# Performance work log

Measured on AMD Instinct MI355X. Metric: run time of the kernel, lower is better.

## Reference

```python
import jax, jax.numpy as jnp
import numpy as np

N, E, G = 100000, 800000, 64
F_IN, H = 92, 4
D1, D2, D3 = 32, 64, 128  # per-head out dims: hidden//2, hidden, 2*hidden
HID, LAT = 64, 128
FINAL = H * D3  # 512
NEG_SLOPE = 0.2


def _p(key, shape, scale=0.05):
    return jax.random.normal(key, shape, dtype=jnp.float32) * scale


def setup_inputs() -> dict:
    key = jax.random.key(0)
    ks = jax.random.split(key, 32)
    node_feat = jax.random.normal(ks[0], (N, F_IN), dtype=jnp.float32)
    src = jax.random.randint(ks[1], (E,), 0, N)
    dst = jax.random.randint(ks[2], (E,), 0, N)
    graph_id = jnp.sort(jax.random.randint(ks[3], (N,), 0, G))
    d = {"node_feat": node_feat, "src": src, "dst": dst, "graph_id": graph_id}
    # GAT layer params (DGL GATConv: fc no bias, attn_l/attn_r [H,D], bias [H*D])
    dims = [(F_IN, D1), (H * D1, D2), (H * D2, D3)]
    i = 4
    for li, (fi, do) in enumerate(dims, 1):
        d[f"W{li}"] = _p(ks[i], (fi, H * do)); i += 1
        d[f"al{li}"] = _p(ks[i], (H, do)); i += 1
        d[f"ar{li}"] = _p(ks[i], (H, do)); i += 1
        d[f"b{li}"] = jnp.zeros((H * do,), dtype=jnp.float32)
    # gate MLP: Linear(final, hid) -> ReLU -> Linear(hid, 1)
    d["Wg1"] = _p(ks[i], (FINAL, HID)); i += 1
    d["bg1"] = jnp.zeros((HID,), dtype=jnp.float32)
    d["Wg2"] = _p(ks[i], (HID, 1)); i += 1
    d["bg2"] = jnp.zeros((1,), dtype=jnp.float32)
    d["Wmu"] = _p(ks[i], (FINAL, LAT)); i += 1
    d["bmu"] = jnp.zeros((LAT,), dtype=jnp.float32)
    d["Wlv"] = _p(ks[i], (FINAL, LAT)); i += 1
    d["blv"] = jnp.zeros((LAT,), dtype=jnp.float32)
    return d


def gat_layer(h, W, al, ar, b, src, dst, heads, d_out):
    n = h.shape[0]
    Wh = (h @ W).reshape(n, heads, d_out)                      # [N,H,D]
    el = jnp.einsum('nhd,hd->nh', Wh, al)                      # a_l . Wh
    er = jnp.einsum('nhd,hd->nh', Wh, ar)
    e = jax.nn.leaky_relu(el[src] + er[dst], NEG_SLOPE)        # [E,H]
    m = jax.ops.segment_max(e, dst, num_segments=n)
    m = jnp.where(jnp.isfinite(m), m, 0.0)                     # zero-in-degree guard
    ex = jnp.exp(e - m[dst])
    s = jax.ops.segment_sum(ex, dst, num_segments=n)
    a = ex / jnp.maximum(s[dst], 1e-9)                         # edge softmax
    msg = a[:, :, None] * Wh[src]                              # [E,H,D] (peak intermediate)
    out = jax.ops.segment_sum(msg, dst, num_segments=n)        # scatter-aggregate
    out = out + b.reshape(1, heads, d_out)
    return out.reshape(n, heads * d_out)                       # flatten(1)


def attention_pool(h, graph_id, Wg1, bg1, Wg2, bg2, num_graphs):
    gate = jax.nn.relu(h @ Wg1 + bg1) @ Wg2 + bg2              # [N,1]
    m = jax.ops.segment_max(gate, graph_id, num_segments=num_graphs)
    ex = jnp.exp(gate - m[graph_id])
    s = jax.ops.segment_sum(ex, graph_id, num_segments=num_graphs)
    a = ex / jnp.maximum(s[graph_id], 1e-9)                    # softmax over nodes per graph
    return jax.ops.segment_sum(a * h, graph_id, num_segments=num_graphs)  # [G,final]


def reference(node_feat, src, dst, graph_id,
              W1, al1, ar1, b1, W2, al2, ar2, b2, W3, al3, ar3, b3,
              Wg1, bg1, Wg2, bg2, Wmu, bmu, Wlv, blv):
    h = jax.nn.elu(gat_layer(node_feat, W1, al1, ar1, b1, src, dst, H, D1))
    h = jax.nn.elu(gat_layer(h, W2, al2, ar2, b2, src, dst, H, D2))
    h = jax.nn.elu(gat_layer(h, W3, al3, ar3, b3, src, dst, H, D3))
    g = attention_pool(h, graph_id, Wg1, bg1, Wg2, bg2, G)
    mu = g @ Wmu + bmu
    logvar = g @ Wlv + blv
    return (mu, logvar)
```

## Files before the change

kernel.cpp:

```cpp
#include <hip/hip_runtime.h>
#include <math.h>

#define NNODES 100000
#define NEDGES 800000
#define NGRAPH 64
#define NHEAD  4
#define FINALD 512
#define HIDG   64
#define LATD   128
#define K1P    96
#define NB_SCAN 98
#define PQ     16

typedef unsigned int uint;
typedef unsigned short ushort;
typedef __attribute__((ext_vector_type(8))) short bf16x8;
typedef __attribute__((ext_vector_type(4))) float f32x4;

__device__ __forceinline__ float bflo(uint u) { return __uint_as_float(u << 16); }
__device__ __forceinline__ float bfhi(uint u) { return __uint_as_float(u & 0xffff0000u); }
__device__ __forceinline__ ushort f2bf(float f) {
    uint u = __float_as_uint(f);
    return (ushort)((u + 0x7fffu + ((u >> 16) & 1u)) >> 16);
}
__device__ __forceinline__ uint pack2(float a, float b) {
    return (uint)f2bf(a) | ((uint)f2bf(b) << 16);
}
__device__ __forceinline__ void fmabf2(float w, uint v, float& a0, float& a1) {
    a0 = fmaf(w, bflo(v), a0);
    a1 = fmaf(w, bfhi(v), a1);
}

__device__ __forceinline__ void async_copy16(const ushort* gsrc, ushort* lds_base) {
    __builtin_amdgcn_global_load_lds(
        (const __attribute__((address_space(1))) uint*)gsrc,
        (__attribute__((address_space(3))) uint*)lds_base,
        16, 0, 0);
}

__global__ void init_kernel(int* __restrict__ deg, const int* __restrict__ gid,
                            int* __restrict__ gstart) {
    int i = blockIdx.x * blockDim.x + threadIdx.x;
    if (i < NNODES) deg[i] = 0;
    if (i <= NGRAPH) {
        int lo = 0, hi = NNODES;
        while (lo < hi) {
            int mid = (lo + hi) >> 1;
            if (gid[mid] < i) lo = mid + 1; else hi = mid;
        }
        gstart[i] = lo;
    }
}
__global__ void count_kernel(const int* __restrict__ dst, int* __restrict__ deg) {
    int e = blockIdx.x * blockDim.x + threadIdx.x;
    if (e < NEDGES) atomicAdd(&deg[dst[e]], 1);
}
__global__ __launch_bounds__(1024) void scan_block_kernel(const int* __restrict__ deg,
                                                          int* __restrict__ off,
                                                          int* __restrict__ bsum) {
    __shared__ int buf[1024];
    int t = threadIdx.x;
    int i = blockIdx.x * 1024 + t;
    int x = (i < NNODES) ? deg[i] : 0;
    buf[t] = x;
    __syncthreads();
    for (int s = 1; s < 1024; s <<= 1) {
        int v = (t >= s) ? buf[t - s] : 0;
        __syncthreads();
        buf[t] += v;
        __syncthreads();
    }
    if (i < NNODES) off[i] = buf[t] - x;
    if (t == 1023) bsum[blockIdx.x] = buf[1023];
}
__global__ __launch_bounds__(128) void scan_bsum_kernel(int* __restrict__ bsum) {
    __shared__ int buf[128];
    int t = threadIdx.x;
    int x = (t < NB_SCAN) ? bsum[t] : 0;
    buf[t] = x;
    __syncthreads();
    for (int s = 1; s < 128; s <<= 1) {
        int v = (t >= s) ? buf[t - s] : 0;
        __syncthreads();
        buf[t] += v;
        __syncthreads();
    }
    if (t < NB_SCAN) bsum[t] = buf[t] - x;
    if (t == 0) bsum[NB_SCAN] = buf[NB_SCAN - 1];
}
__global__ __launch_bounds__(1024) void scan_add_kernel(int* __restrict__ off,
                                                        const int* __restrict__ bsum,
                                                        int* __restrict__ cursor) {
    int i = blockIdx.x * 1024 + threadIdx.x;
    if (i < NNODES) {
        int v = off[i] + bsum[blockIdx.x];
        off[i] = v;
        cursor[i] = v;
    }
    if (i == 0) off[NNODES] = bsum[NB_SCAN];
}
__global__ void scatter_kernel(const int* __restrict__ src, const int* __restrict__ dst,
                               int* __restrict__ cursor, int* __restrict__ src_csr) {
    int e = blockIdx.x * blockDim.x + threadIdx.x;
    if (e >= NEDGES) return;
    int p = atomicAdd(&cursor[dst[e]], 1);
    src_csr[p] = src[e];
}

#define C1 (128 * K1P)
#define C2 (256 * 128)
#define C3 (512 * 256)
#define CG (64 * 512)
#define CX (NNODES * K1P)
#define CTOT (C1 + C2 + C3 + CG + CX + NNODES)
__global__ void conv_all_kernel(const float* __restrict__ W1, const float* __restrict__ W2,
                                const float* __restrict__ W3, const float* __restrict__ Wg1,
                                const float* __restrict__ nf,
                                ushort* __restrict__ Bt1, ushort* __restrict__ Bt2,
                                ushort* __restrict__ Bt3, ushort* __restrict__ Btg,
                                ushort* __restrict__ x0, float* __restrict__ gate) {
    int i = blockIdx.x * blockDim.x + threadIdx.x;
    if (i < C1) {
        int n = i / K1P, k = i - n * K1P;
        Bt1[i] = (k < 92) ? f2bf(W1[(size_t)k * 128 + n]) : (ushort)0;
        return;
    }
    i -= C1;
    if (i < C2) {
        int n = i >> 7, k = i & 127;
        Bt2[i] = f2bf(W2[(size_t)k * 256 + n]);
        return;
    }
    i -= C2;
    if (i < C3) {
        int n = i >> 8, k = i & 255;
        Bt3[i] = f2bf(W3[(size_t)k * 512 + n]);
        return;
    }
    i -= C3;
    if (i < CG) {
        int n = i >> 9, k = i & 511;
        Btg[i] = f2bf(Wg1[(size_t)k * 64 + n]);
        return;
    }
    i -= CG;
    if (i < CX) {
        int n = i / K1P, k = i - n * K1P;
        x0[i] = (k < 92) ? f2bf(nf[(size_t)n * 92 + k]) : (ushort)0;
        return;
    }
    i -= CX;
    if (i < NNODES) gate[i] = 0.f;
}

template <int BN, int MODE>
__global__ __launch_bounds__(256) void mfma_gemm(const ushort* __restrict__ A,
                                                 const ushort* __restrict__ Bt,
                                                 const float* __restrict__ bias,
                                                 ushort* __restrict__ C,
                                                 const float* __restrict__ Wg2,
                                                 float* __restrict__ gate,
                                                 int M, int K, int N) {
    constexpr int WNS = BN / 2;
    constexpr int NT = WNS / 16;
    __shared__ ushort Alds[128][32];
    __shared__ ushort Blds[BN][32];
    int tid = threadIdx.x;
    int wave = tid >> 6, lane = tid & 63;
    int wm = wave & 1, wn = wave >> 1;
    int quad = lane >> 4, l16 = lane & 15;
    int rowBase = blockIdx.y * 128;
    int colBase = blockIdx.x * BN;

    int srow = lane >> 2;
    int scol = (lane & 3) * 8;

    f32x4 acc[4][NT];
#pragma unroll
    for (int i = 0; i < 4; i++)
#pragma unroll
        for (int j = 0; j < NT; j++) acc[i][j] = (f32x4){0.f, 0.f, 0.f, 0.f};

    for (int k0 = 0; k0 < K; k0 += 32) {
#pragma unroll
        for (int c = 0; c < 2; c++) {
            int chunk = wave * 2 + c;
            int row = rowBase + chunk * 16 + srow;
            async_copy16(&A[(size_t)row * K + k0 + scol], &Alds[chunk * 16][0]);
        }
        if constexpr (BN == 128) {
#pragma unroll
            for (int c = 0; c < 2; c++) {
                int chunk = wave * 2 + c;
                int row = colBase + chunk * 16 + srow;
                async_copy16(&Bt[(size_t)row * K + k0 + scol], &Blds[chunk * 16][0]);
            }
        } else {
            int row = colBase + wave * 16 + srow;
            async_copy16(&Bt[(size_t)row * K + k0 + scol], &Blds[wave * 16][0]);
        }
        __syncthreads();
        bf16x8 af[4], bf[NT];
#pragma unroll
        for (int i = 0; i < 4; i++)
            af[i] = *(const bf16x8*)&Alds[wm * 64 + i * 16 + l16][quad * 8];
#pragma unroll
        for (int j = 0; j < NT; j++)
            bf[j] = *(const bf16x8*)&Blds[wn * WNS + j * 16 + l16][quad * 8];
#pragma unroll
        for (int i = 0; i < 4; i++)
#pragma unroll
            for (int j = 0; j < NT; j++)
                acc[i][j] = __builtin_amdgcn_mfma_f32_16x16x32_bf16(af[i], bf[j], acc[i][j], 0, 0, 0);
        __syncthreads();
    }

    if constexpr (MODE == 0) {
#pragma unroll
        for (int i = 0; i < 4; i++) {
#pragma unroll
            for (int j = 0; j < NT; j++) {
                int col = colBase + wn * WNS + j * 16 + l16;
#pragma unroll
                for (int r = 0; r < 4; r++) {
                    int row = rowBase + wm * 64 + i * 16 + quad * 4 + r;
                    if (row < M) C[(size_t)row * N + col] = f2bf(acc[i][j][r]);
                }
            }
        }
    } else {
        float bb[NT], wg[NT];
#pragma unroll
        for (int j = 0; j < NT; j++) {
            int col = colBase + wn * WNS + j * 16 + l16;
            bb[j] = bias[col];
            wg[j] = Wg2[col];
        }
#pragma unroll
        for (int i = 0; i < 4; i++) {
            float pd[4] = {0.f, 0.f, 0.f, 0.f};
#pragma unroll
            for (int j = 0; j < NT; j++) {
#pragma unroll
                for (int r = 0; r < 4; r++) {
                    float x = fmaxf(acc[i][j][r] + bb[j], 0.f);
                    pd[r] = fmaf(x, wg[j], pd[r]);
                }
            }
#pragma unroll
            for (int m = 1; m < 16; m <<= 1)
#pragma unroll
                for (int r = 0; r < 4; r++)
                    pd[r] += __shfl_xor(pd[r], m, 64);
            if (l16 == 0) {
#pragma unroll
                for (int r = 0; r < 4; r++) {
                    int row = rowBase + wm * 64 + i * 16 + quad * 4 + r;
                    if (row < M) atomicAdd(&gate[row], pd[r]);
                }
            }
        }
    }
}

template <int HD>
__global__ __launch_bounds__(256) void eler_node(const ushort* __restrict__ Wh,
                                                 const float* __restrict__ al,
                                                 const float* __restrict__ ar,
                                                 float* __restrict__ el,
                                                 float* __restrict__ er) {
    constexpr int LPN = HD / 8;
    constexpr int NPW = 64 / LPN;
    constexpr int S = (HD / NHEAD) / 8;
    int wave = threadIdx.x >> 6;
    int lane = threadIdx.x & 63;
    int sub = lane & (LPN - 1);
    int n = blockIdx.x * (4 * NPW) + wave * NPW + lane / LPN;
    int d0 = sub * 8;
    uint4 v = *(const uint4*)&Wh[(size_t)n * HD + d0];
    float w0 = bflo(v.x), w1 = bfhi(v.x), w2 = bflo(v.y), w3 = bfhi(v.y);
    float w4 = bflo(v.z), w5 = bfhi(v.z), w6 = bflo(v.w), w7 = bfhi(v.w);
    float4 a0 = *(const float4*)&al[d0];
    float4 a1 = *(const float4*)&al[d0 + 4];
    float4 b0 = *(const float4*)&ar[d0];
    float4 b1 = *(const float4*)&ar[d0 + 4];
    float sl, sr;
    sl = w0 * a0.x; sl = fmaf(w1, a0.y, sl); sl = fmaf(w2, a0.z, sl); sl = fmaf(w3, a0.w, sl);
    sl = fmaf(w4, a1.x, sl); sl = fmaf(w5, a1.y, sl); sl = fmaf(w6, a1.z, sl); sl = fmaf(w7, a1.w, sl);
    sr = w0 * b0.x; sr = fmaf(w1, b0.y, sr); sr = fmaf(w2, b0.z, sr); sr = fmaf(w3, b0.w, sr);
    sr = fmaf(w4, b1.x, sr); sr = fmaf(w5, b1.y, sr); sr = fmaf(w6, b1.z, sr); sr = fmaf(w7, b1.w, sr);
#pragma unroll
    for (int o = S / 2; o > 0; o >>= 1) {
        sl += __shfl_down(sl, o, 64);
        sr += __shfl_down(sr, o, 64);
    }
    if ((sub & (S - 1)) == 0) {
        int h = sub / S;
        el[n * 4 + h] = sl;
        er[n * 4 + h] = sr;
    }
}

__global__ void attn_node(const int* __restrict__ src_csr, const int* __restrict__ off,
                          const float4* __restrict__ el4, const float4* __restrict__ er4,
                          float4* __restrict__ aw4, float4* __restrict__ nsum4) {
    int n = blockIdx.x * blockDim.x + threadIdx.x;
    if (n >= NNODES) return;
    int i0 = off[n], i1 = off[n + 1];
    float4 ern = er4[n];
    float m0 = -1e30f, m1 = -1e30f, m2 = -1e30f, m3 = -1e30f;
    for (int i = i0; i < i1; i += 8) {
        int cnt = i1 - i; if (cnt > 8) cnt = 8;
        int s8[8];
#pragma unroll
        for (int j = 0; j < 8; j++)
            if (j < cnt) s8[j] = src_csr[i + j];
        float4 e8[8];
#pragma unroll
        for (int j = 0; j < 8; j++)
            if (j < cnt) e8[j] = el4[s8[j]];
#pragma unroll
        for (int j = 0; j < 8; j++) {
            if (j < cnt) {
                float4 x = e8[j];
                x.x += ern.x; x.y += ern.y; x.z += ern.z; x.w += ern.w;
                x.x = (x.x >= 0.f) ? x.x : 0.2f * x.x;
                x.y = (x.y >= 0.f) ? x.y : 0.2f * x.y;
                x.z = (x.z >= 0.f) ? x.z : 0.2f * x.z;
                x.w = (x.w >= 0.f) ? x.w : 0.2f * x.w;
                aw4[i + j] = x;
                m0 = fmaxf(m0, x.x); m1 = fmaxf(m1, x.y);
                m2 = fmaxf(m2, x.z); m3 = fmaxf(m3, x.w);
            }
        }
    }
    float4 s = make_float4(0.f, 0.f, 0.f, 0.f);
    for (int i = i0; i < i1; i++) {
        float4 x = aw4[i];
        x.x = expf(x.x - m0); x.y = expf(x.y - m1);
        x.z = expf(x.z - m2); x.w = expf(x.w - m3);
        s.x += x.x; s.y += x.y; s.z += x.z; s.w += x.w;
        aw4[i] = x;
    }
    nsum4[n] = s;
}

template <int HD, int DPL>
__global__ __launch_bounds__(256) void gat_aggregate2(const int* __restrict__ src_csr,
                                                      const int* __restrict__ off,
                                                      const ushort* __restrict__ Wh,
                                                      const float* __restrict__ aw,
                                                      const float* __restrict__ nsum,
                                                      const float* __restrict__ bias,
                                                      ushort* __restrict__ out,
                                                      int pass) {
    constexpr int LOGD = (HD == 128) ? 5 : (HD == 256) ? 6 : 7;
    const int lane = threadIdx.x & 63;
    const int wv = __builtin_amdgcn_readfirstlane((int)(threadIdx.x >> 6));
    const int n = blockIdx.x * 4 + wv;
    const int d = pass * (64 * DPL) + lane * DPL;
    const int h = d >> LOGD;
    const int i0 = __builtin_amdgcn_readfirstlane(off[n]);
    const int i1 = __builtin_amdgcn_readfirstlane(off[n + 1]);

    float a0 = 0.f, a1 = 0.f, a2 = 0.f, a3 = 0.f;
    const ushort* __restrict__ col = Wh + d;

    int i = i0;
    for (; i + 4 <= i1; i += 4) {
        const int s0 = __builtin_amdgcn_readfirstlane(src_csr[i + 0]);
        const int s1 = __builtin_amdgcn_readfirstlane(src_csr[i + 1]);
        const int s2 = __builtin_amdgcn_readfirstlane(src_csr[i + 2]);
        const int s3 = __builtin_amdgcn_readfirstlane(src_csr[i + 3]);
        const float w0 = aw[(i + 0) * 4 + h];
        const float w1 = aw[(i + 1) * 4 + h];
        const float w2 = aw[(i + 2) * 4 + h];
        const float w3 = aw[(i + 3) * 4 + h];
        if constexpr (DPL == 4) {
            uint2 v0 = *(const uint2*)&col[(size_t)s0 * HD];
            uint2 v1 = *(const uint2*)&col[(size_t)s1 * HD];
            uint2 v2 = *(const uint2*)&col[(size_t)s2 * HD];
            uint2 v3 = *(const uint2*)&col[(size_t)s3 * HD];
            fmabf2(w0, v0.x, a0, a1); fmabf2(w0, v0.y, a2, a3);
            fmabf2(w1, v1.x, a0, a1); fmabf2(w1, v1.y, a2, a3);
            fmabf2(w2, v2.x, a0, a1); fmabf2(w2, v2.y, a2, a3);
            fmabf2(w3, v3.x, a0, a1); fmabf2(w3, v3.y, a2, a3);
        } else {
            uint v0 = *(const uint*)&col[(size_t)s0 * HD];
            uint v1 = *(const uint*)&col[(size_t)s1 * HD];
            uint v2 = *(const uint*)&col[(size_t)s2 * HD];
            uint v3 = *(const uint*)&col[(size_t)s3 * HD];
            fmabf2(w0, v0, a0, a1);
            fmabf2(w1, v1, a0, a1);
            fmabf2(w2, v2, a0, a1);
            fmabf2(w3, v3, a0, a1);
        }
    }
    for (; i < i1; ++i) {
        const int s0 = __builtin_amdgcn_readfirstlane(src_csr[i]);
        const float w0 = aw[i * 4 + h];
        if constexpr (DPL == 4) {
            uint2 v0 = *(const uint2*)&col[(size_t)s0 * HD];
            fmabf2(w0, v0.x, a0, a1); fmabf2(w0, v0.y, a2, a3);
        } else {
            uint v0 = *(const uint*)&col[(size_t)s0 * HD];
            fmabf2(w0, v0, a0, a1);
        }
    }

    const float inv = 1.f / fmaxf(nsum[n * 4 + h], 1e-9f);
    float x0 = a0 * inv + bias[d + 0];
    float x1 = a1 * inv + bias[d + 1];
    x0 = (x0 > 0.f) ? x0 : (expf(x0) - 1.f);
    x1 = (x1 > 0.f) ? x1 : (expf(x1) - 1.f);
    if constexpr (DPL == 4) {
        float x2 = a2 * inv + bias[d + 2];
        float x3 = a3 * inv + bias[d + 3];
        x2 = (x2 > 0.f) ? x2 : (expf(x2) - 1.f);
        x3 = (x3 > 0.f) ? x3 : (expf(x3) - 1.f);
        uint2 o;
        o.x = pack2(x0, x1);
        o.y = pack2(x2, x3);
        *(uint2*)&out[(size_t)n * HD + d] = o;
    } else {
        *(uint*)&out[(size_t)n * HD + d] = pack2(x0, x1);
    }
}

__global__ __launch_bounds__(256) void graph_softmax_kernel(const float* __restrict__ gate,
                                                            const int* __restrict__ gstart,
                                                            float* __restrict__ exn,
                                                            float* __restrict__ gsum) {
    int g = blockIdx.x, t = threadIdx.x;
    int n0 = gstart[g], n1 = gstart[g + 1];
    __shared__ float red[256];
    float m = -1e30f;
    for (int n = n0 + t; n < n1; n += 256) m = fmaxf(m, gate[n]);
    red[t] = m; __syncthreads();
    for (int s = 128; s > 0; s >>= 1) {
        if (t < s) red[t] = fmaxf(red[t], red[t + s]);
        __syncthreads();
    }
    m = red[0]; __syncthreads();
    float sum = 0.f;
    for (int n = n0 + t; n < n1; n += 256) {
        float v = expf(gate[n] - m);
        exn[n] = v;
        sum += v;
    }
    red[t] = sum; __syncthreads();
    for (int s = 128; s > 0; s >>= 1) {
        if (t < s) red[t] += red[t + s];
        __syncthreads();
    }
    if (t == 0) gsum[g] = red[0];
}

__global__ __launch_bounds__(128) void pool_partial(const ushort* __restrict__ h,
                                                    const float* __restrict__ exn,
                                                    const int* __restrict__ gstart,
                                                    float* __restrict__ partial) {
    int g = blockIdx.x, q = blockIdx.y;
    int n0 = gstart[g], n1 = gstart[g + 1];
    int len = n1 - n0;
    int chunk = (len + PQ - 1) / PQ;
    int s = n0 + q * chunk;
    int e = s + chunk; if (e > n1) e = n1;
    int d4 = threadIdx.x;
    const uint2* h2 = (const uint2*)h;
    float a0 = 0.f, a1 = 0.f, a2 = 0.f, a3 = 0.f;
    for (int n = s; n < e; n++) {
        float w = exn[n];
        uint2 v = h2[(size_t)n * 128 + d4];
        a0 = fmaf(w, bflo(v.x), a0);
        a1 = fmaf(w, bfhi(v.x), a1);
        a2 = fmaf(w, bflo(v.y), a2);
        a3 = fmaf(w, bfhi(v.y), a3);
    }
    *(float4*)&partial[((size_t)(g * PQ + q)) * FINALD + d4 * 4] = make_float4(a0, a1, a2, a3);
}

__global__ __launch_bounds__(128) void final_kernel(const float* __restrict__ partial,
                                                    const float* __restrict__ gsum,
                                                    const float* __restrict__ Wmu,
                                                    const float* __restrict__ bmu,
                                                    const float* __restrict__ Wlv,
                                                    const float* __restrict__ blv,
                                                    float* __restrict__ out) {
    int g = blockIdx.x, j = threadIdx.x;
    __shared__ float pooled[FINALD];
    const float* p = partial + (size_t)g * PQ * FINALD;
    for (int k = j; k < FINALD; k += 128) {
        float v = 0.f;
#pragma unroll
        for (int q = 0; q < PQ; q++) v += p[q * FINALD + k];
        pooled[k] = v;
    }
    __syncthreads();
    float am = 0.f, av = 0.f;
    for (int k = 0; k < FINALD; k++) {
        float pv = pooled[k];
        am = fmaf(pv, Wmu[k * LATD + j], am);
        av = fmaf(pv, Wlv[k * LATD + j], av);
    }
    float inv = 1.f / fmaxf(gsum[g], 1e-9f);
    out[g * LATD + j] = am * inv + bmu[j];
    out[NGRAPH * LATD + g * LATD + j] = av * inv + blv[j];
}

extern "C" void kernel_launch(void* const* d_in, const int* in_sizes, int n_in,
                              void* d_out, int out_size, void* d_ws, size_t ws_size,
                              hipStream_t stream) {
    (void)in_sizes; (void)n_in; (void)out_size; (void)ws_size;
    const float* node_feat = (const float*)d_in[0];
    const int* src = (const int*)d_in[1];
    const int* dst = (const int*)d_in[2];
    const int* gid = (const int*)d_in[3];
    const float* W[3]    = {(const float*)d_in[4],  (const float*)d_in[8],  (const float*)d_in[12]};
    const float* al[3]   = {(const float*)d_in[5],  (const float*)d_in[9],  (const float*)d_in[13]};
    const float* ar[3]   = {(const float*)d_in[6],  (const float*)d_in[10], (const float*)d_in[14]};
    const float* bias[3] = {(const float*)d_in[7],  (const float*)d_in[11], (const float*)d_in[15]};
    const float* Wg1 = (const float*)d_in[16];
    const float* bg1 = (const float*)d_in[17];
    const float* Wg2 = (const float*)d_in[18];
    const float* Wmu = (const float*)d_in[20];
    const float* bmu = (const float*)d_in[21];
    const float* Wlv = (const float*)d_in[22];
    const float* blv = (const float*)d_in[23];

    char* ws = (char*)d_ws;
    size_t woff = 0;
    auto carve = [&](size_t bytes) {
        void* p = ws + woff;
        woff = (woff + bytes + 255) & ~(size_t)255;
        return p;
    };
    ushort* hA      = (ushort*)carve((size_t)NNODES * 512 * 2);
    ushort* hB      = (ushort*)carve((size_t)NNODES * 512 * 2);
    float*  el      = (float*) carve((size_t)NNODES * 4 * 4);
    float*  er      = (float*) carve((size_t)NNODES * 4 * 4);
    float*  aw      = (float*) carve((size_t)NEDGES * 4 * 4);
    float*  nsum    = (float*) carve((size_t)NNODES * 4 * 4);
    int*    deg     = (int*)   carve((size_t)NNODES * 4);
    int*    off     = (int*)   carve((size_t)(NNODES + 1) * 4);
    int*    cursor  = (int*)   carve((size_t)NNODES * 4);
    int*    src_csr = (int*)   carve((size_t)NEDGES * 4);
    int*    bsum    = (int*)   carve((size_t)(NB_SCAN + 1) * 4);
    float*  gate    = (float*) carve((size_t)NNODES * 4);
    float*  exn     = (float*) carve((size_t)NNODES * 4);
    int*    gstart  = (int*)   carve((size_t)(NGRAPH + 1) * 4);
    float*  partial = (float*) carve((size_t)NGRAPH * PQ * FINALD * 4);
    float*  gsum    = (float*) carve((size_t)NGRAPH * 4);
    ushort* Bt1     = (ushort*)carve((size_t)128 * K1P * 2);
    ushort* Bt2     = (ushort*)carve((size_t)256 * 128 * 2);
    ushort* Bt3     = (ushort*)carve((size_t)512 * 256 * 2);
    ushort* Btg     = (ushort*)carve((size_t)64 * 512 * 2 + 4096);
    ushort* x0      = hA;

    init_kernel<<<(NNODES + 255) / 256, 256, 0, stream>>>(deg, gid, gstart);
    count_kernel<<<(NEDGES + 255) / 256, 256, 0, stream>>>(dst, deg);
    scan_block_kernel<<<NB_SCAN, 1024, 0, stream>>>(deg, off, bsum);
    scan_bsum_kernel<<<1, 128, 0, stream>>>(bsum);
    scan_add_kernel<<<NB_SCAN, 1024, 0, stream>>>(off, bsum, cursor);
    scatter_kernel<<<(NEDGES + 255) / 256, 256, 0, stream>>>(src, dst, cursor, src_csr);
    conv_all_kernel<<<(CTOT + 255) / 256, 256, 0, stream>>>(
        W[0], W[1], W[2], Wg1, node_feat, Bt1, Bt2, Bt3, Btg, x0, gate);

    const int MB = (NNODES + 127) / 128;
    const int AGB = NNODES / 4;

    mfma_gemm<128, 0><<<dim3(1, MB), 256, 0, stream>>>(
        x0, Bt1, nullptr, hB, nullptr, nullptr, NNODES, K1P, 128);
    eler_node<128><<<NNODES / 16, 256, 0, stream>>>(hB, al[0], ar[0], el, er);
    attn_node<<<(NNODES + 255) / 256, 256, 0, stream>>>(
        src_csr, off, (const float4*)el, (const float4*)er, (float4*)aw, (float4*)nsum);
    gat_aggregate2<128, 2><<<AGB, 256, 0, stream>>>(
        src_csr, off, hB, aw, nsum, bias[0], hA, 0);

    mfma_gemm<128, 0><<<dim3(2, MB), 256, 0, stream>>>(
        hA, Bt2, nullptr, hB, nullptr, nullptr, NNODES, 128, 256);
    eler_node<256><<<NNODES / 8, 256, 0, stream>>>(hB, al[1], ar[1], el, er);
    attn_node<<<(NNODES + 255) / 256, 256, 0, stream>>>(
        src_csr, off, (const float4*)el, (const float4*)er, (float4*)aw, (float4*)nsum);
    gat_aggregate2<256, 4><<<AGB, 256, 0, stream>>>(
        src_csr, off, hB, aw, nsum, bias[1], hA, 0);

    mfma_gemm<128, 0><<<dim3(4, MB), 256, 0, stream>>>(
        hA, Bt3, nullptr, hB, nullptr, nullptr, NNODES, 256, 512);
    eler_node<512><<<NNODES / 4, 256, 0, stream>>>(hB, al[2], ar[2], el, er);
    attn_node<<<(NNODES + 255) / 256, 256, 0, stream>>>(
        src_csr, off, (const float4*)el, (const float4*)er, (float4*)aw, (float4*)nsum);
    gat_aggregate2<512, 4><<<AGB, 256, 0, stream>>>(
        src_csr, off, hB, aw, nsum, bias[2], hA, 0);
    gat_aggregate2<512, 4><<<AGB, 256, 0, stream>>>(
        src_csr, off, hB, aw, nsum, bias[2], hA, 1);

    mfma_gemm<64, 1><<<dim3(1, MB), 256, 0, stream>>>(
        hA, Btg, bg1, nullptr, Wg2, gate, NNODES, FINALD, HIDG);
    graph_softmax_kernel<<<NGRAPH, 256, 0, stream>>>(gate, gstart, exn, gsum);
    pool_partial<<<dim3(NGRAPH, PQ), 128, 0, stream>>>(hA, exn, gstart, partial);
    final_kernel<<<NGRAPH, 128, 0, stream>>>(partial, gsum, Wmu, bmu, Wlv, blv, (float*)d_out);
}
```

Baseline: 771.0 us.

## Fuse el/er attention logits into GEMM epilogue and widen aggregation batching

Removes the separate eler_node kernels and computes the per-head a_l·Wh and a_r·Wh dot products inside the MFMA GEMM epilogue, reducing fp32 accumulators across lanes and atomically adding them into el/er. The el/er buffers are zeroed first in the conversion kernel and then by the aggregation kernel for the next layer. The aggregation kernel is generalised to a batch size B of edges and a variable lanes-per-node width. The last layer now covers all 512 columns with 8 elements per lane in a single pass instead of two passes. This avoids rereading Wh for the logits and saves launches, at the cost of atomics, an epilogue that reads fp32 accumulators rather than rounded bf16, and more registers.

```diff
diff --git a/kernel.cpp b/kernel.cpp
--- a/kernel.cpp
+++ b/kernel.cpp
@@ -112,13 +112,15 @@
 #define C3 (512 * 256)
 #define CG (64 * 512)
 #define CX (NNODES * K1P)
-#define CTOT (C1 + C2 + C3 + CG + CX + NNODES)
+#define CEL (NNODES * 4)
+#define CTOT (C1 + C2 + C3 + CG + CX + NNODES + 2 * CEL)
 __global__ void conv_all_kernel(const float* __restrict__ W1, const float* __restrict__ W2,
                                 const float* __restrict__ W3, const float* __restrict__ Wg1,
                                 const float* __restrict__ nf,
                                 ushort* __restrict__ Bt1, ushort* __restrict__ Bt2,
                                 ushort* __restrict__ Bt3, ushort* __restrict__ Btg,
-                                ushort* __restrict__ x0, float* __restrict__ gate) {
+                                ushort* __restrict__ x0, float* __restrict__ gate,
+                                float* __restrict__ el, float* __restrict__ er) {
     int i = blockIdx.x * blockDim.x + threadIdx.x;
     if (i < C1) {
         int n = i / K1P, k = i - n * K1P;
@@ -150,16 +152,24 @@
         return;
     }
     i -= CX;
-    if (i < NNODES) gate[i] = 0.f;
-}
-
-template <int BN, int MODE>
+    if (i < NNODES) { gate[i] = 0.f; return; }
+    i -= NNODES;
+    if (i < CEL) { el[i] = 0.f; return; }
+    i -= CEL;
+    if (i < CEL) er[i] = 0.f;
+}
+
+template <int BN, int MODE, int LOGD>
 __global__ __launch_bounds__(256) void mfma_gemm(const ushort* __restrict__ A,
                                                  const ushort* __restrict__ Bt,
                                                  const float* __restrict__ bias,
                                                  ushort* __restrict__ C,
                                                  const float* __restrict__ Wg2,
                                                  float* __restrict__ gate,
+                                                 const float* __restrict__ al,
+                                                 const float* __restrict__ ar,
+                                                 float* __restrict__ elp,
+                                                 float* __restrict__ erp,
                                                  int M, int K, int N) {
     constexpr int WNS = BN / 2;
     constexpr int NT = WNS / 16;
@@ -228,6 +238,57 @@
                 }
             }
         }
+        constexpr int NGt = WNS >> LOGD;
+        constexpr int NG = (NGt < 1) ? 1 : NGt;
+        constexpr int SH = LOGD - 4;
+        float alv[NT], arv[NT];
+#pragma unroll
+        for (int j = 0; j < NT; j++) {
+            int col = colBase + wn * WNS + j * 16 + l16;
+            alv[j] = al[col];
+            arv[j] = ar[col];
+        }
+        int h0 = (colBase + wn * WNS) >> LOGD;
+#pragma unroll
+        for (int i = 0; i < 4; i++) {
+            float pl[NG][4], pr[NG][4];
+#pragma unroll
+            for (int g = 0; g < NG; g++)
+#pragma unroll
+                for (int r = 0; r < 4; r++) { pl[g][r] = 0.f; pr[g][r] = 0.f; }
+#pragma unroll
+            for (int j = 0; j < NT; j++) {
+                constexpr int dummy = 0; (void)dummy;
+                int g = (NG == 1) ? 0 : (j >> SH);
+#pragma unroll
+                for (int r = 0; r < 4; r++) {
+                    pl[g][r] = fmaf(acc[i][j][r], alv[j], pl[g][r]);
+                    pr[g][r] = fmaf(acc[i][j][r], arv[j], pr[g][r]);
+                }
+            }
+#pragma unroll
+            for (int m = 1; m < 16; m <<= 1)
+#pragma unroll
+                for (int g = 0; g < NG; g++)
+#pragma unroll
+                    for (int r = 0; r < 4; r++) {
+                        pl[g][r] += __shfl_xor(pl[g][r], m, 64);
+                        pr[g][r] += __shfl_xor(pr[g][r], m, 64);
+                    }
+            if (l16 == 0) {
+#pragma unroll
+                for (int r = 0; r < 4; r++) {
+                    int row = rowBase + wm * 64 + i * 16 + quad * 4 + r;
+                    if (row < M) {
+#pragma unroll
+                        for (int g = 0; g < NG; g++) {
+                            atomicAdd(&elp[row * 4 + h0 + g], pl[g][r]);
+                            atomicAdd(&erp[row * 4 + h0 + g], pr[g][r]);
+                        }
+                    }
+                }
+            }
+        }
     } else {
         float bb[NT], wg[NT];
 #pragma unroll
@@ -260,44 +321,6 @@
                 }
             }
         }
-    }
-}
-
-template <int HD>
-__global__ __launch_bounds__(256) void eler_node(const ushort* __restrict__ Wh,
-                                                 const float* __restrict__ al,
-                                                 const float* __restrict__ ar,
-                                                 float* __restrict__ el,
-                                                 float* __restrict__ er) {
-    constexpr int LPN = HD / 8;
-    constexpr int NPW = 64 / LPN;
-    constexpr int S = (HD / NHEAD) / 8;
-    int wave = threadIdx.x >> 6;
-    int lane = threadIdx.x & 63;
-    int sub = lane & (LPN - 1);
-    int n = blockIdx.x * (4 * NPW) + wave * NPW + lane / LPN;
-    int d0 = sub * 8;
-    uint4 v = *(const uint4*)&Wh[(size_t)n * HD + d0];
-    float w0 = bflo(v.x), w1 = bfhi(v.x), w2 = bflo(v.y), w3 = bfhi(v.y);
-    float w4 = bflo(v.z), w5 = bfhi(v.z), w6 = bflo(v.w), w7 = bfhi(v.w);
-    float4 a0 = *(const float4*)&al[d0];
-    float4 a1 = *(const float4*)&al[d0 + 4];
-    float4 b0 = *(const float4*)&ar[d0];
-    float4 b1 = *(const float4*)&ar[d0 + 4];
-    float sl, sr;
-    sl = w0 * a0.x; sl = fmaf(w1, a0.y, sl); sl = fmaf(w2, a0.z, sl); sl = fmaf(w3, a0.w, sl);
-    sl = fmaf(w4, a1.x, sl); sl = fmaf(w5, a1.y, sl); sl = fmaf(w6, a1.z, sl); sl = fmaf(w7, a1.w, sl);
-    sr = w0 * b0.x; sr = fmaf(w1, b0.y, sr); sr = fmaf(w2, b0.z, sr); sr = fmaf(w3, b0.w, sr);
-    sr = fmaf(w4, b1.x, sr); sr = fmaf(w5, b1.y, sr); sr = fmaf(w6, b1.z, sr); sr = fmaf(w7, b1.w, sr);
-#pragma unroll
-    for (int o = S / 2; o > 0; o >>= 1) {
-        sl += __shfl_down(sl, o, 64);
-        sr += __shfl_down(sr, o, 64);
-    }
-    if ((sub & (S - 1)) == 0) {
-        int h = sub / S;
-        el[n * 4 + h] = sl;
-        er[n * 4 + h] = sr;
     }
 }
 
@@ -345,86 +368,107 @@
     nsum4[n] = s;
 }
 
-template <int HD, int DPL>
-__global__ __launch_bounds__(256) void gat_aggregate2(const int* __restrict__ src_csr,
+template <int HD, int DPL, int B>
+__global__ __launch_bounds__(256) void gat_aggregate3(const int* __restrict__ src_csr,
                                                       const int* __restrict__ off,
                                                       const ushort* __restrict__ Wh,
                                                       const float* __restrict__ aw,
                                                       const float* __restrict__ nsum,
                                                       const float* __restrict__ bias,
                                                       ushort* __restrict__ out,
-                                                      int pass) {
+                                                      float* __restrict__ elz,
+                                                      float* __restrict__ erz) {
     constexpr int LOGD = (HD == 128) ? 5 : (HD == 256) ? 6 : 7;
     const int lane = threadIdx.x & 63;
     const int wv = __builtin_amdgcn_readfirstlane((int)(threadIdx.x >> 6));
     const int n = blockIdx.x * 4 + wv;
-    const int d = pass * (64 * DPL) + lane * DPL;
+    const int d = lane * DPL;
     const int h = d >> LOGD;
     const int i0 = __builtin_amdgcn_readfirstlane(off[n]);
     const int i1 = __builtin_amdgcn_readfirstlane(off[n + 1]);
 
-    float a0 = 0.f, a1 = 0.f, a2 = 0.f, a3 = 0.f;
+    float acc[DPL];
+#pragma unroll
+    for (int j = 0; j < DPL; j++) acc[j] = 0.f;
     const ushort* __restrict__ col = Wh + d;
 
     int i = i0;
-    for (; i + 4 <= i1; i += 4) {
-        const int s0 = __builtin_amdgcn_readfirstlane(src_csr[i + 0]);
-        const int s1 = __builtin_amdgcn_readfirstlane(src_csr[i + 1]);
-        const int s2 = __builtin_amdgcn_readfirstlane(src_csr[i + 2]);
-        const int s3 = __builtin_amdgcn_readfirstlane(src_csr[i + 3]);
-        const float w0 = aw[(i + 0) * 4 + h];
-        const float w1 = aw[(i + 1) * 4 + h];
-        const float w2 = aw[(i + 2) * 4 + h];
-        const float w3 = aw[(i + 3) * 4 + h];
-        if constexpr (DPL == 4) {
+    for (; i + B <= i1; i += B) {
+        int s[B];
+        float w[B];
+#pragma unroll
+        for (int b = 0; b < B; b++) s[b] = __builtin_amdgcn_readfirstlane(src_csr[i + b]);
+#pragma unroll
+        for (int b = 0; b < B; b++) w[b] = aw[(size_t)(i + b) * 4 + h];
+        if constexpr (DPL == 8) {
+            uint4 v[B];
+#pragma unroll
+            for (int b = 0; b < B; b++) v[b] = *(const uint4*)&col[(size_t)s[b] * HD];
+#pragma unroll
+            for (int b = 0; b < B; b++) {
+                fmabf2(w[b], v[b].x, acc[0], acc[1]);
+                fmabf2(w[b], v[b].y, acc[2], acc[3]);
+                fmabf2(w[b], v[b].z, acc[4], acc[5]);
+                fmabf2(w[b], v[b].w, acc[6], acc[7]);
+            }
+        } else if constexpr (DPL == 4) {
+            uint2 v[B];
+#pragma unroll
+            for (int b = 0; b < B; b++) v[b] = *(const uint2*)&col[(size_t)s[b] * HD];
+#pragma unroll
+            for (int b = 0; b < B; b++) {
+                fmabf2(w[b], v[b].x, acc[0], acc[1]);
+                fmabf2(w[b], v[b].y, acc[2], acc[3]);
+            }
+        } else {
+            uint v[B];
+#pragma unroll
+            for (int b = 0; b < B; b++) v[b] = *(const uint*)&col[(size_t)s[b] * HD];
+#pragma unroll
+            for (int b = 0; b < B; b++) fmabf2(w[b], v[b], acc[0], acc[1]);
+        }
+    }
+    for (; i < i1; ++i) {
+        const int s0 = __builtin_amdgcn_readfirstlane(src_csr[i]);
+        const float w0 = aw[(size_t)i * 4 + h];
+        if constexpr (DPL == 8) {
+            uint4 v0 = *(const uint4*)&col[(size_t)s0 * HD];
+            fmabf2(w0, v0.x, acc[0], acc[1]);
+            fmabf2(w0, v0.y, acc[2], acc[3]);
+            fmabf2(w0, v0.z, acc[4], acc[5]);
+            fmabf2(w0, v0.w, acc[6], acc[7]);
+        } else if constexpr (DPL == 4) {
             uint2 v0 = *(const uint2*)&col[(size_t)s0 * HD];
-            uint2 v1 = *(const uint2*)&col[(size_t)s1 * HD];
-            uint2 v2 = *(const uint2*)&col[(size_t)s2 * HD];
-            uint2 v3 = *(const uint2*)&col[(size_t)s3 * HD];
-            fmabf2(w0, v0.x, a0, a1); fmabf2(w0, v0.y, a2, a3);
-            fmabf2(w1, v1.x, a0, a1); fmabf2(w1, v1.y, a2, a3);
-            fmabf2(w2, v2.x, a0, a1); fmabf2(w2, v2.y, a2, a3);
-            fmabf2(w3, v3.x, a0, a1); fmabf2(w3, v3.y, a2, a3);
+            fmabf2(w0, v0.x, acc[0], acc[1]);
+            fmabf2(w0, v0.y, acc[2], acc[3]);
         } else {
             uint v0 = *(const uint*)&col[(size_t)s0 * HD];
-            uint v1 = *(const uint*)&col[(size_t)s1 * HD];
-            uint v2 = *(const uint*)&col[(size_t)s2 * HD];
-            uint v3 = *(const uint*)&col[(size_t)s3 * HD];
-            fmabf2(w0, v0, a0, a1);
-            fmabf2(w1, v1, a0, a1);
-            fmabf2(w2, v2, a0, a1);
-            fmabf2(w3, v3, a0, a1);
-        }
-    }
-    for (; i < i1; ++i) {
-        const int s0 = __builtin_amdgcn_readfirstlane(src_csr[i]);
-        const float w0 = aw[i * 4 + h];
-        if constexpr (DPL == 4) {
-            uint2 v0 = *(const uint2*)&col[(size_t)s0 * HD];
-            fmabf2(w0, v0.x, a0, a1); fmabf2(w0, v0.y, a2, a3);
-        } else {
-            uint v0 = *(const uint*)&col[(size_t)s0 * HD];
-            fmabf2(w0, v0, a0, a1);
+            fmabf2(w0, v0, acc[0], acc[1]);
         }
     }
 
     const float inv = 1.f / fmaxf(nsum[n * 4 + h], 1e-9f);
-    float x0 = a0 * inv + bias[d + 0];
-    float x1 = a1 * inv + bias[d + 1];
-    x0 = (x0 > 0.f) ? x0 : (expf(x0) - 1.f);
-    x1 = (x1 > 0.f) ? x1 : (expf(x1) - 1.f);
-    if constexpr (DPL == 4) {
-        float x2 = a2 * inv + bias[d + 2];
-        float x3 = a3 * inv + bias[d + 3];
-        x2 = (x2 > 0.f) ? x2 : (expf(x2) - 1.f);
-        x3 = (x3 > 0.f) ? x3 : (expf(x3) - 1.f);
+    float x[DPL];
+#pragma unroll
+    for (int j = 0; j < DPL; j++) {
+        float v = acc[j] * inv + bias[d + j];
+        x[j] = (v > 0.f) ? v : (expf(v) - 1.f);
+    }
+    if constexpr (DPL == 8) {
+        uint4 o;
+        o.x = pack2(x[0], x[1]); o.y = pack2(x[2], x[3]);
+        o.z = pack2(x[4], x[5]); o.w = pack2(x[6], x[7]);
+        *(uint4*)&out[(size_t)n * HD + d] = o;
+    } else if constexpr (DPL == 4) {
         uint2 o;
-        o.x = pack2(x0, x1);
-        o.y = pack2(x2, x3);
+        o.x = pack2(x[0], x[1]); o.y = pack2(x[2], x[3]);
         *(uint2*)&out[(size_t)n * HD + d] = o;
     } else {
-        *(uint*)&out[(size_t)n * HD + d] = pack2(x0, x1);
-    }
+        *(uint*)&out[(size_t)n * HD + d] = pack2(x[0], x[1]);
+    }
+
+    if (lane < 4) elz[n * 4 + lane] = 0.f;
+    else if (lane < 8) erz[n * 4 + (lane - 4)] = 0.f;
 }
 
 __global__ __launch_bounds__(256) void graph_softmax_kernel(const float* __restrict__ gate,
@@ -564,39 +608,34 @@
     scan_add_kernel<<<NB_SCAN, 1024, 0, stream>>>(off, bsum, cursor);
     scatter_kernel<<<(NEDGES + 255) / 256, 256, 0, stream>>>(src, dst, cursor, src_csr);
     conv_all_kernel<<<(CTOT + 255) / 256, 256, 0, stream>>>(
-        W[0], W[1], W[2], Wg1, node_feat, Bt1, Bt2, Bt3, Btg, x0, gate);
+        W[0], W[1], W[2], Wg1, node_feat, Bt1, Bt2, Bt3, Btg, x0, gate, el, er);
 
     const int MB = (NNODES + 127) / 128;
     const int AGB = NNODES / 4;
 
-    mfma_gemm<128, 0><<<dim3(1, MB), 256, 0, stream>>>(
-        x0, Bt1, nullptr, hB, nullptr, nullptr, NNODES, K1P, 128);
-    eler_node<128><<<NNODES / 16, 256, 0, stream>>>(hB, al[0], ar[0], el, er);
+    mfma_gemm<128, 0, 5><<<dim3(1, MB), 256, 0, stream>>>(
+        x0, Bt1, nullptr, hB, nullptr, nullptr, al[0], ar[0], el, er, NNODES, K1P, 128);
     attn_node<<<(NNODES + 255) / 256, 256, 0, stream>>>(
         src_csr, off, (const float4*)el, (const float4*)er, (float4*)aw, (float4*)nsum);
-    gat_aggregate2<128, 2><<<AGB, 256, 0, stream>>>(
-        src_csr, off, hB, aw, nsum, bias[0], hA, 0);
-
-    mfma_gemm<128, 0><<<dim3(2, MB), 256, 0, stream>>>(
-        hA, Bt2, nullptr, hB, nullptr, nullptr, NNODES, 128, 256);
-    eler_node<256><<<NNODES / 8, 256, 0, stream>>>(hB, al[1], ar[1], el, er);
+    gat_aggregate3<128, 2, 8><<<AGB, 256, 0, stream>>>(
+        src_csr, off, hB, aw, nsum, bias[0], hA, el, er);
+
+    mfma_gemm<128, 0, 6><<<dim3(2, MB), 256, 0, stream>>>(
+        hA, Bt2, nullptr, hB, nullptr, nullptr, al[1], ar[1], el, er, NNODES, 128, 256);
     attn_node<<<(NNODES + 255) / 256, 256, 0, stream>>>(
         src_csr, off, (const float4*)el, (const float4*)er, (float4*)aw, (float4*)nsum);
-    gat_aggregate2<256, 4><<<AGB, 256, 0, stream>>>(
-        src_csr, off, hB, aw, nsum, bias[1], hA, 0);
-
-    mfma_gemm<128, 0><<<dim3(4, MB), 256, 0, stream>>>(
-        hA, Bt3, nullptr, hB, nullptr, nullptr, NNODES, 256, 512);
-    eler_node<512><<<NNODES / 4, 256, 0, stream>>>(hB, al[2], ar[2], el, er);
+    gat_aggregate3<256, 4, 8><<<AGB, 256, 0, stream>>>(
+        src_csr, off, hB, aw, nsum, bias[1], hA, el, er);
+
+    mfma_gemm<128, 0, 7><<<dim3(4, MB), 256, 0, stream>>>(
+        hA, Bt3, nullptr, hB, nullptr, nullptr, al[2], ar[2], el, er, NNODES, 256, 512);
     attn_node<<<(NNODES + 255) / 256, 256, 0, stream>>>(
         src_csr, off, (const float4*)el, (const float4*)er, (float4*)aw, (float4*)nsum);
-    gat_aggregate2<512, 4><<<AGB, 256, 0, stream>>>(
-        src_csr, off, hB, aw, nsum, bias[2], hA, 0);
-    gat_aggregate2<512, 4><<<AGB, 256, 0, stream>>>(
-        src_csr, off, hB, aw, nsum, bias[2], hA, 1);
-
-    mfma_gemm<64, 1><<<dim3(1, MB), 256, 0, stream>>>(
-        hA, Btg, bg1, nullptr, Wg2, gate, NNODES, FINALD, HIDG);
+    gat_aggregate3<512, 8, 4><<<AGB, 256, 0, stream>>>(
+        src_csr, off, hB, aw, nsum, bias[2], hA, el, er);
+
+    mfma_gemm<64, 1, 0><<<dim3(1, MB), 256, 0, stream>>>(
+        hA, Btg, bg1, nullptr, Wg2, gate, nullptr, nullptr, nullptr, nullptr, NNODES, FINALD, HIDG);
     graph_softmax_kernel<<<NGRAPH, 256, 0, stream>>>(gate, gstart, exn, gsum);
     pool_partial<<<dim3(NGRAPH, PQ), 128, 0, stream>>>(hA, exn, gstart, partial);
     final_kernel<<<NGRAPH, 128, 0, stream>>>(partial, gsum, Wmu, bmu, Wlv, blv, (float*)d_out);
```

After: 890.1 us. 15.4% more time.

## Fuse softmax exponent and normalizer into aggregation, unroll edges by eight

Applied to the files above, without the earlier changes.

attn_node now writes only the raw leaky-relu scores and the per-node per-head max, dropping its second pass that re-read and rewrote every edge weight with exp and summed them. The aggregation kernel computes exp(score - max) per edge on the fly, accumulates the softmax denominator itself, and batches eight edges per iteration instead of four so more gathers are in flight. This removes a read-modify-write pass over the edge weight array per layer. In exchange, exp is recomputed in every aggregation lane and pass (twice for the final layer), and register pressure rises from the larger unroll.

```diff
diff --git a/kernel.cpp b/kernel.cpp
--- a/kernel.cpp
+++ b/kernel.cpp
@@ -303,7 +303,7 @@
 
 __global__ void attn_node(const int* __restrict__ src_csr, const int* __restrict__ off,
                           const float4* __restrict__ el4, const float4* __restrict__ er4,
-                          float4* __restrict__ aw4, float4* __restrict__ nsum4) {
+                          float4* __restrict__ aw4, float4* __restrict__ m4) {
     int n = blockIdx.x * blockDim.x + threadIdx.x;
     if (n >= NNODES) return;
     int i0 = off[n], i1 = off[n + 1];
@@ -334,23 +334,15 @@
             }
         }
     }
-    float4 s = make_float4(0.f, 0.f, 0.f, 0.f);
-    for (int i = i0; i < i1; i++) {
-        float4 x = aw4[i];
-        x.x = expf(x.x - m0); x.y = expf(x.y - m1);
-        x.z = expf(x.z - m2); x.w = expf(x.w - m3);
-        s.x += x.x; s.y += x.y; s.z += x.z; s.w += x.w;
-        aw4[i] = x;
-    }
-    nsum4[n] = s;
-}
-
-template <int HD, int DPL>
-__global__ __launch_bounds__(256) void gat_aggregate2(const int* __restrict__ src_csr,
+    m4[n] = make_float4(m0, m1, m2, m3);
+}
+
+template <int HD, int DPL, int B>
+__global__ __launch_bounds__(256) void gat_aggregate4(const int* __restrict__ src_csr,
                                                       const int* __restrict__ off,
                                                       const ushort* __restrict__ Wh,
                                                       const float* __restrict__ aw,
-                                                      const float* __restrict__ nsum,
+                                                      const float* __restrict__ m4,
                                                       const float* __restrict__ bias,
                                                       ushort* __restrict__ out,
                                                       int pass) {
@@ -362,68 +354,93 @@
     const int h = d >> LOGD;
     const int i0 = __builtin_amdgcn_readfirstlane(off[n]);
     const int i1 = __builtin_amdgcn_readfirstlane(off[n + 1]);
-
-    float a0 = 0.f, a1 = 0.f, a2 = 0.f, a3 = 0.f;
+    const float mh = m4[n * 4 + h];
+
+    float acc[DPL];
+#pragma unroll
+    for (int j = 0; j < DPL; j++) acc[j] = 0.f;
+    float ssum = 0.f;
     const ushort* __restrict__ col = Wh + d;
 
     int i = i0;
-    for (; i + 4 <= i1; i += 4) {
-        const int s0 = __builtin_amdgcn_readfirstlane(src_csr[i + 0]);
-        const int s1 = __builtin_amdgcn_readfirstlane(src_csr[i + 1]);
-        const int s2 = __builtin_amdgcn_readfirstlane(src_csr[i + 2]);
-        const int s3 = __builtin_amdgcn_readfirstlane(src_csr[i + 3]);
-        const float w0 = aw[(i + 0) * 4 + h];
-        const float w1 = aw[(i + 1) * 4 + h];
-        const float w2 = aw[(i + 2) * 4 + h];
-        const float w3 = aw[(i + 3) * 4 + h];
-        if constexpr (DPL == 4) {
+    for (; i + B <= i1; i += B) {
+        int s[B];
+        float w[B];
+#pragma unroll
+        for (int b = 0; b < B; b++) s[b] = __builtin_amdgcn_readfirstlane(src_csr[i + b]);
+#pragma unroll
+        for (int b = 0; b < B; b++) w[b] = expf(aw[(size_t)(i + b) * 4 + h] - mh);
+        if constexpr (DPL == 8) {
+            uint4 v[B];
+#pragma unroll
+            for (int b = 0; b < B; b++) v[b] = *(const uint4*)&col[(size_t)s[b] * HD];
+#pragma unroll
+            for (int b = 0; b < B; b++) {
+                ssum += w[b];
+                fmabf2(w[b], v[b].x, acc[0], acc[1]);
+                fmabf2(w[b], v[b].y, acc[2], acc[3]);
+                fmabf2(w[b], v[b].z, acc[4], acc[5]);
+                fmabf2(w[b], v[b].w, acc[6], acc[7]);
+            }
+        } else if constexpr (DPL == 4) {
+            uint2 v[B];
+#pragma unroll
+            for (int b = 0; b < B; b++) v[b] = *(const uint2*)&col[(size_t)s[b] * HD];
+#pragma unroll
+            for (int b = 0; b < B; b++) {
+                ssum += w[b];
+                fmabf2(w[b], v[b].x, acc[0], acc[1]);
+                fmabf2(w[b], v[b].y, acc[2], acc[3]);
+            }
+        } else {
+            uint v[B];
+#pragma unroll
+            for (int b = 0; b < B; b++) v[b] = *(const uint*)&col[(size_t)s[b] * HD];
+#pragma unroll
+            for (int b = 0; b < B; b++) {
+                ssum += w[b];
+                fmabf2(w[b], v[b], acc[0], acc[1]);
+            }
+        }
+    }
+    for (; i < i1; ++i) {
+        const int s0 = __builtin_amdgcn_readfirstlane(src_csr[i]);
+        const float w0 = expf(aw[(size_t)i * 4 + h] - mh);
+        ssum += w0;
+        if constexpr (DPL == 8) {
+            uint4 v0 = *(const uint4*)&col[(size_t)s0 * HD];
+            fmabf2(w0, v0.x, acc[0], acc[1]);
+            fmabf2(w0, v0.y, acc[2], acc[3]);
+            fmabf2(w0, v0.z, acc[4], acc[5]);
+            fmabf2(w0, v0.w, acc[6], acc[7]);
+        } else if constexpr (DPL == 4) {
             uint2 v0 = *(const uint2*)&col[(size_t)s0 * HD];
-            uint2 v1 = *(const uint2*)&col[(size_t)s1 * HD];
-            uint2 v2 = *(const uint2*)&col[(size_t)s2 * HD];
-            uint2 v3 = *(const uint2*)&col[(size_t)s3 * HD];
-            fmabf2(w0, v0.x, a0, a1); fmabf2(w0, v0.y, a2, a3);
-            fmabf2(w1, v1.x, a0, a1); fmabf2(w1, v1.y, a2, a3);
-            fmabf2(w2, v2.x, a0, a1); fmabf2(w2, v2.y, a2, a3);
-            fmabf2(w3, v3.x, a0, a1); fmabf2(w3, v3.y, a2, a3);
+            fmabf2(w0, v0.x, acc[0], acc[1]);
+            fmabf2(w0, v0.y, acc[2], acc[3]);
         } else {
             uint v0 = *(const uint*)&col[(size_t)s0 * HD];
-            uint v1 = *(const uint*)&col[(size_t)s1 * HD];
-            uint v2 = *(const uint*)&col[(size_t)s2 * HD];
-            uint v3 = *(const uint*)&col[(size_t)s3 * HD];
-            fmabf2(w0, v0, a0, a1);
-            fmabf2(w1, v1, a0, a1);
-            fmabf2(w2, v2, a0, a1);
-            fmabf2(w3, v3, a0, a1);
-        }
-    }
-    for (; i < i1; ++i) {
-        const int s0 = __builtin_amdgcn_readfirstlane(src_csr[i]);
-        const float w0 = aw[i * 4 + h];
-        if constexpr (DPL == 4) {
-            uint2 v0 = *(const uint2*)&col[(size_t)s0 * HD];
-            fmabf2(w0, v0.x, a0, a1); fmabf2(w0, v0.y, a2, a3);
-        } else {
-            uint v0 = *(const uint*)&col[(size_t)s0 * HD];
-            fmabf2(w0, v0, a0, a1);
-        }
-    }
-
-    const float inv = 1.f / fmaxf(nsum[n * 4 + h], 1e-9f);
-    float x0 = a0 * inv + bias[d + 0];
-    float x1 = a1 * inv + bias[d + 1];
-    x0 = (x0 > 0.f) ? x0 : (expf(x0) - 1.f);
-    x1 = (x1 > 0.f) ? x1 : (expf(x1) - 1.f);
-    if constexpr (DPL == 4) {
-        float x2 = a2 * inv + bias[d + 2];
-        float x3 = a3 * inv + bias[d + 3];
-        x2 = (x2 > 0.f) ? x2 : (expf(x2) - 1.f);
-        x3 = (x3 > 0.f) ? x3 : (expf(x3) - 1.f);
+            fmabf2(w0, v0, acc[0], acc[1]);
+        }
+    }
+
+    const float inv = 1.f / fmaxf(ssum, 1e-9f);
+    float x[DPL];
+#pragma unroll
+    for (int j = 0; j < DPL; j++) {
+        float v = acc[j] * inv + bias[d + j];
+        x[j] = (v > 0.f) ? v : (expf(v) - 1.f);
+    }
+    if constexpr (DPL == 8) {
+        uint4 o;
+        o.x = pack2(x[0], x[1]); o.y = pack2(x[2], x[3]);
+        o.z = pack2(x[4], x[5]); o.w = pack2(x[6], x[7]);
+        *(uint4*)&out[(size_t)n * HD + d] = o;
+    } else if constexpr (DPL == 4) {
         uint2 o;
-        o.x = pack2(x0, x1);
-        o.y = pack2(x2, x3);
+        o.x = pack2(x[0], x[1]); o.y = pack2(x[2], x[3]);
         *(uint2*)&out[(size_t)n * HD + d] = o;
     } else {
-        *(uint*)&out[(size_t)n * HD + d] = pack2(x0, x1);
+        *(uint*)&out[(size_t)n * HD + d] = pack2(x[0], x[1]);
     }
 }
 
@@ -540,7 +557,7 @@
     float*  el      = (float*) carve((size_t)NNODES * 4 * 4);
     float*  er      = (float*) carve((size_t)NNODES * 4 * 4);
     float*  aw      = (float*) carve((size_t)NEDGES * 4 * 4);
-    float*  nsum    = (float*) carve((size_t)NNODES * 4 * 4);
+    float*  m4      = (float*) carve((size_t)NNODES * 4 * 4);
     int*    deg     = (int*)   carve((size_t)NNODES * 4);
     int*    off     = (int*)   carve((size_t)(NNODES + 1) * 4);
     int*    cursor  = (int*)   carve((size_t)NNODES * 4);
@@ -573,27 +590,27 @@
         x0, Bt1, nullptr, hB, nullptr, nullptr, NNODES, K1P, 128);
     eler_node<128><<<NNODES / 16, 256, 0, stream>>>(hB, al[0], ar[0], el, er);
     attn_node<<<(NNODES + 255) / 256, 256, 0, stream>>>(
-        src_csr, off, (const float4*)el, (const float4*)er, (float4*)aw, (float4*)nsum);
-    gat_aggregate2<128, 2><<<AGB, 256, 0, stream>>>(
-        src_csr, off, hB, aw, nsum, bias[0], hA, 0);
+        src_csr, off, (const float4*)el, (const float4*)er, (float4*)aw, (float4*)m4);
+    gat_aggregate4<128, 2, 8><<<AGB, 256, 0, stream>>>(
+        src_csr, off, hB, aw, m4, bias[0], hA, 0);
 
     mfma_gemm<128, 0><<<dim3(2, MB), 256, 0, stream>>>(
         hA, Bt2, nullptr, hB, nullptr, nullptr, NNODES, 128, 256);
     eler_node<256><<<NNODES / 8, 256, 0, stream>>>(hB, al[1], ar[1], el, er);
     attn_node<<<(NNODES + 255) / 256, 256, 0, stream>>>(
-        src_csr, off, (const float4*)el, (const float4*)er, (float4*)aw, (float4*)nsum);
-    gat_aggregate2<256, 4><<<AGB, 256, 0, stream>>>(
-        src_csr, off, hB, aw, nsum, bias[1], hA, 0);
+        src_csr, off, (const float4*)el, (const float4*)er, (float4*)aw, (float4*)m4);
+    gat_aggregate4<256, 4, 8><<<AGB, 256, 0, stream>>>(
+        src_csr, off, hB, aw, m4, bias[1], hA, 0);
 
     mfma_gemm<128, 0><<<dim3(4, MB), 256, 0, stream>>>(
         hA, Bt3, nullptr, hB, nullptr, nullptr, NNODES, 256, 512);
     eler_node<512><<<NNODES / 4, 256, 0, stream>>>(hB, al[2], ar[2], el, er);
     attn_node<<<(NNODES + 255) / 256, 256, 0, stream>>>(
-        src_csr, off, (const float4*)el, (const float4*)er, (float4*)aw, (float4*)nsum);
-    gat_aggregate2<512, 4><<<AGB, 256, 0, stream>>>(
-        src_csr, off, hB, aw, nsum, bias[2], hA, 0);
-    gat_aggregate2<512, 4><<<AGB, 256, 0, stream>>>(
-        src_csr, off, hB, aw, nsum, bias[2], hA, 1);
+        src_csr, off, (const float4*)el, (const float4*)er, (float4*)aw, (float4*)m4);
+    gat_aggregate4<512, 4, 8><<<AGB, 256, 0, stream>>>(
+        src_csr, off, hB, aw, m4, bias[2], hA, 0);
+    gat_aggregate4<512, 4, 8><<<AGB, 256, 0, stream>>>(
+        src_csr, off, hB, aw, m4, bias[2], hA, 1);
 
     mfma_gemm<64, 1><<<dim3(1, MB), 256, 0, stream>>>(
         hA, Btg, bg1, nullptr, Wg2, gate, NNODES, FINALD, HIDG);
```

Result: no change. 774.2 us (+0.4%).
